# Kernel tuning notes

Measured on AMD Instinct MI355X. Metric: run time of the kernel, lower is better.

## Reference

```python
import jax, jax.numpy as jnp
import numpy as np

EMBED = 768; HEADS = 12; MLP = 3072
WL_IN = 4        # activation bits (signed)
WL_W = 4         # weight bits (bit-sliced into 1-bit RRAM cells)
ADC = 5          # ADC precision for each analog partial sum
SUBARRAY = 128   # crossbar subArray rows
ONOFF = 10.0     # conductance on/off ratio
VARI = 0.02      # conductance variability
EPS = 1e-5


def _adc_quant(y, bits):
    # Linear ADC quantization over the full observed range.
    ymax = jnp.max(jnp.abs(y))
    step = ymax / (2 ** bits - 1)
    step = jnp.where(step > 0, step, jnp.ones_like(step))
    return jnp.round(y / step) * step


def _qlinear(x, W, b, key):
    # RRAM crossbar simulated linear layer. x: [T, Fin], W: [Fout, Fin].
    upper, lower = 1.0, 1.0 / ONOFF
    T, Fin = x.shape
    Fout = W.shape[0]
    Wlev = 2 ** WL_W - 1
    Xlev = 2 ** (WL_IN - 1) - 1
    # --- weight -> unsigned integer levels -> binary cell conductances ---
    wmax = jnp.max(jnp.abs(W))
    Wdec = jnp.round((W / wmax + 1.0) * 0.5 * Wlev).astype(jnp.int32)   # [Fout,Fin] in [0,Wlev]
    kb = jnp.arange(WL_W)
    wbits = ((Wdec[:, :, None] >> kb) & 1).astype(x.dtype)              # [Fout,Fin,K]
    noise = VARI * jax.random.normal(key, wbits.shape, dtype=x.dtype)   # conductance variability
    cond = (wbits * (upper - lower) + lower) * (1.0 + noise)
    dummy = 0.5 * (upper + lower)                                       # dummy column conductance
    # --- activation -> signed integer -> magnitude bit slices ---
    xmax = jnp.max(jnp.abs(x))
    Xq = jnp.round(x / xmax * Xlev).astype(jnp.int32)
    sgn = jnp.sign(Xq).astype(x.dtype)
    zb = jnp.arange(WL_IN - 1)
    xbits = ((jnp.abs(Xq)[:, :, None] >> zb) & 1).astype(x.dtype) * sgn[:, :, None]  # [T,Fin,Z]
    # --- subArray partitioning along input dim ---
    pad = (-Fin) % SUBARRAY
    if pad:
        xbits = jnp.pad(xbits, ((0, 0), (0, pad), (0, 0)))
        cond = jnp.pad(cond, ((0, 0), (0, pad), (0, 0)))
    nc = (Fin + pad) // SUBARRAY
    xb = xbits.reshape(T, nc, SUBARRAY, WL_IN - 1)
    cb = cond.reshape(Fout, nc, SUBARRAY, WL_W)
    # analog MAC per subarray, per (input bit z, weight cell k)
    partial = jnp.einsum('tcsz,ocsk->tcozk', xb, cb)                    # [T,nc,Fout,Z,K]
    dummyP = dummy * xb.sum(axis=2)                                     # [T,nc,Z]
    partialQ = _adc_quant(partial, ADC)
    dummyQ = _adc_quant(dummyP, ADC)
    net = partialQ - dummyQ[:, :, None, :, None]                        # recenter to signed weights
    scale = (2.0 ** zb)[:, None] * (2.0 ** kb)[None, :]                 # [Z,K] shift-add
    acc = jnp.einsum('tcozk,zk->to', net, scale)
    out = acc * (xmax / Xlev) * (2.0 * wmax / ((upper - lower) * Wlev))
    return out + b


def _layernorm(x, g, b):
    mu = jnp.mean(x, axis=-1, keepdims=True)
    var = jnp.var(x, axis=-1, keepdims=True)
    return (x - mu) * jax.lax.rsqrt(var + EPS) * g + b


def _attention(x, in_w, in_b, out_w, out_b):
    L, N, E = x.shape
    D = E // HEADS
    qkv = x @ in_w.T + in_b                                             # [L,N,3E]
    q, k, v = jnp.split(qkv, 3, axis=-1)
    q = q.reshape(L, N, HEADS, D)
    k = k.reshape(L, N, HEADS, D)
    v = v.reshape(L, N, HEADS, D)
    scores = jnp.einsum('lnhd,mnhd->nhlm', q, k) / jnp.sqrt(jnp.asarray(D, x.dtype))
    attn = jax.nn.softmax(scores, axis=-1)
    ctx = jnp.einsum('nhlm,mnhd->lnhd', attn, v).reshape(L, N, E)
    return ctx @ out_w.T + out_b


def setup_inputs() -> dict:
    key = jax.random.key(0)
    ks = jax.random.split(key, 8)
    s = 0.02
    return {
        'x': jax.random.normal(ks[0], (256, 2, EMBED), jnp.float32),
        'in_proj_w': s * jax.random.normal(ks[1], (3 * EMBED, EMBED), jnp.float32),
        'in_proj_b': jnp.zeros((3 * EMBED,), jnp.float32),
        'out_proj_w': s * jax.random.normal(ks[2], (EMBED, EMBED), jnp.float32),
        'out_proj_b': jnp.zeros((EMBED,), jnp.float32),
        'ln1_g': jnp.ones((EMBED,), jnp.float32),
        'ln1_b': jnp.zeros((EMBED,), jnp.float32),
        'W1': s * jax.random.normal(ks[3], (MLP, EMBED), jnp.float32),
        'b1': jnp.zeros((MLP,), jnp.float32),
        'W2': s * jax.random.normal(ks[4], (EMBED, MLP), jnp.float32),
        'b2': jnp.zeros((EMBED,), jnp.float32),
        'ln2_g': jnp.ones((EMBED,), jnp.float32),
        'ln2_b': jnp.zeros((EMBED,), jnp.float32),
    }


def reference(x, in_proj_w, in_proj_b, out_proj_w, out_proj_b,
              ln1_g, ln1_b, W1, b1, W2, b2, ln2_g, ln2_b):
    L, N, E = x.shape
    a = _attention(x, in_proj_w, in_proj_b, out_proj_w, out_proj_b)
    h = _layernorm(x + a, ln1_g, ln1_b)
    t = h.reshape(L * N, E)
    m = _qlinear(t, W1, b1, jax.random.key(1))
    m = jax.nn.gelu(m, approximate=False)   # torch nn.GELU default = exact erf
    m = _qlinear(m, W2, b2, jax.random.key(2))
    m = m.reshape(L, N, E)
    return _layernorm(h + m, ln2_g, ln2_b)
```

## Files before the change

kernel.cpp:

```cpp
#include <hip/hip_runtime.h>
#include <math.h>
#include <stdint.h>

#define TOK   512
#define EMB   768
#define QKVD  2304
#define NHEAD 12
#define HD    64
#define MLPD  3072
#define SUBA  128

#define OFF_SCAL     0ull
#define OFF_QKV      256ull
#define OFF_SCORES   (OFF_QKV    + 4718592ull)
#define OFF_CTX      (OFF_SCORES + 6291456ull)
#define OFF_H1PRE    (OFF_CTX    + 1572864ull)
#define OFF_H1       (OFF_H1PRE  + 1572864ull)
#define OFF_M1       (OFF_H1     + 1572864ull)
#define OFF_X2       (OFF_M1     + 6291456ull)
#define OFF_M2       (OFF_X2     + 6291456ull)
#define OFF_DQ1      (OFF_M2     + 1572864ull)
#define OFF_DQ2      (OFF_DQ1    + 36864ull)
#define OFF_SUMXB1   (OFF_DQ2    + 147456ull)
#define OFF_SUMXB2   (OFF_SUMXB1 + 36864ull)
#define OFF_WDEC1    (OFF_SUMXB2 + 147456ull)
#define OFF_WDEC2    (OFF_WDEC1  + 2359296ull)
#define OFF_XQT1     (OFF_WDEC2  + 2359296ull)
#define OFF_XQT2     (OFF_XQT1   + 393216ull)
#define OFF_COND1    (OFF_XQT2   + 1572864ull)
#define OFF_COND2    (OFF_COND1  + 37748736ull)
#define WS_NEEDED    (OFF_COND2  + 37748736ull)


typedef float f32x2 __attribute__((ext_vector_type(2)));

__device__ __forceinline__ f32x2 pkfma(f32x2 a, f32x2 b, f32x2 c){
  f32x2 d;
  asm("v_pk_fma_f32 %0, %1, %2, %3" : "=v"(d) : "v"(a), "v"(b), "v"(c));
  return d;
}

__device__ __forceinline__ void blockMaxAtomic(double v, unsigned long long* slot, double* red){
  int tid = threadIdx.x;
  red[tid] = v; __syncthreads();
  for (int st = 128; st > 0; st >>= 1){
    if (tid < st){ double o = red[tid+st]; if (o > red[tid]) red[tid] = o; }
    __syncthreads();
  }
  if (tid == 0) atomicMax(slot, (unsigned long long)__double_as_longlong(red[0]));
}

__device__ __forceinline__ double readSlot(const unsigned long long* s){
  return __longlong_as_double((long long)(*s));
}

__device__ __forceinline__ float xla_exp_f32(float _x){
  float x = fminf(_x, 88.3762626647950f);
  x = fmaxf(x, -88.3762626647949f);
  float m = floorf(fmaf(x, 1.44269504088896341f, 0.5f));
  float r = fmaf(m, -0.6931471805599453f, x);
  float r2 = __fmul_rn(r, r);
  float r3 = __fmul_rn(r2, r);
  float y  = fmaf(1.9875691500e-4f, r, 1.3981999507e-3f);
  float y1 = fmaf(4.1665795894e-2f, r, 1.6666665459e-1f);
  float y2 = __fadd_rn(r, 1.0f);
  y  = fmaf(y, r, 8.3334519073e-3f);
  y1 = fmaf(y1, r, 5.0000001201e-1f);
  y  = fmaf(y, r3, y1);
  y  = fmaf(y, r2, y2);
  int mi = (int)m;
  float two_m = __uint_as_float((unsigned)((mi + 127) << 23));
  float res = __fmul_rn(y, two_m);
  return fmaxf(res, _x);
}

__device__ __forceinline__ float xla_erf_f32(float v){
  float x = fmaxf(fminf(v, 4.0f), -4.0f);
  float x2 = __fmul_rn(x, x);
  float p = fmaf(x2, -2.72614225801306e-10f, 2.77068142495902e-08f);
  p = fmaf(x2, p, -2.10102402082508e-06f);
  p = fmaf(x2, p, -5.69250639462346e-05f);
  p = fmaf(x2, p, -7.34990630326855e-04f);
  p = fmaf(x2, p, -2.95459980854025e-03f);
  p = fmaf(x2, p, -1.60960333262415e-02f);
  p = __fmul_rn(x, p);
  float q = fmaf(x2, -1.45660718464996e-05f, -2.13374055278905e-04f);
  q = fmaf(x2, q, -1.68282697438203e-03f);
  q = fmaf(x2, q, -7.37332916720468e-03f);
  q = fmaf(x2, q, -1.42647390514189e-02f);
  return __fdiv_rn(p, q);
}

__device__ __forceinline__ uint32_t rotl32(uint32_t x, int r){ return (x << r) | (x >> (32 - r)); }

__device__ __forceinline__ void threefry2x32(uint32_t k0, uint32_t k1,
                                             uint32_t x0, uint32_t x1,
                                             uint32_t& o0, uint32_t& o1){
  uint32_t ks2 = k0 ^ k1 ^ 0x1BD11BDAu;
  x0 += k0; x1 += k1;
#define TF_R(r) { x0 += x1; x1 = rotl32(x1, r); x1 ^= x0; }
  TF_R(13) TF_R(15) TF_R(26) TF_R(6)
  x0 += k1; x1 += ks2 + 1u;
  TF_R(17) TF_R(29) TF_R(16) TF_R(24)
  x0 += ks2; x1 += k0 + 2u;
  TF_R(13) TF_R(15) TF_R(26) TF_R(6)
  x0 += k0; x1 += k1 + 3u;
  TF_R(17) TF_R(29) TF_R(16) TF_R(24)
  x0 += k1; x1 += ks2 + 4u;
  TF_R(13) TF_R(15) TF_R(26) TF_R(6)
  x0 += ks2; x1 += k0 + 5u;
#undef TF_R
  o0 = x0; o1 = x1;
}

__device__ float bits_to_noise(uint32_t bits){
  uint32_t fb = (bits >> 9) | 0x3f800000u;
  float f = __uint_as_float(fb);
  f = __fadd_rn(f, -1.0f);
  const float lo = -0.99999994f;
  float u = __fadd_rn(__fmul_rn(f, 2.0f), lo);
  u = fmaxf(lo, u);
  float x  = u;
  float xx = __fmul_rn(x, x);
  float nx = -xx;
  float l1p;
  if (fabsf(nx) < 1e-4f){
    l1p = __fmul_rn(__fadd_rn(__fmul_rn(-0.5f, nx), 1.0f), nx);
  } else {
    float u1 = __fadd_rn(nx, 1.0f);
    l1p = (float)log((double)u1);
  }
  float w = -l1p;
  float p;
  if (w < 5.0f){
    w = __fadd_rn(w, -2.5f);
    p = 2.81022636e-08f;
    p = __fadd_rn(3.43273939e-07f, __fmul_rn(p, w));
    p = __fadd_rn(-3.5233877e-06f,  __fmul_rn(p, w));
    p = __fadd_rn(-4.39150654e-06f, __fmul_rn(p, w));
    p = __fadd_rn(0.00021858087f,   __fmul_rn(p, w));
    p = __fadd_rn(-0.00125372503f,  __fmul_rn(p, w));
    p = __fadd_rn(-0.00417768164f,  __fmul_rn(p, w));
    p = __fadd_rn(0.246640727f,     __fmul_rn(p, w));
    p = __fadd_rn(1.50140941f,      __fmul_rn(p, w));
  } else {
    float sw = __fsqrt_rn(w);
    w = __fadd_rn(sw, -3.0f);
    p = -0.000200214257f;
    p = __fadd_rn(0.000100950558f, __fmul_rn(p, w));
    p = __fadd_rn(0.00134934322f,  __fmul_rn(p, w));
    p = __fadd_rn(-0.00367342844f, __fmul_rn(p, w));
    p = __fadd_rn(0.00573950773f,  __fmul_rn(p, w));
    p = __fadd_rn(-0.0076224613f,  __fmul_rn(p, w));
    p = __fadd_rn(0.00943887047f,  __fmul_rn(p, w));
    p = __fadd_rn(1.00167406f,     __fmul_rn(p, w));
    p = __fadd_rn(2.83297682f,     __fmul_rn(p, w));
  }
  float ei  = __fmul_rn(p, x);
  float nrm = __fmul_rn(1.41421354f, ei);
  return __fmul_rn(0.02f, nrm);
}

__global__ void absmax_f32_k(const float* p, int n, unsigned long long* slot){
  __shared__ double red[256];
  double m = 0.0;
  for (int i = blockIdx.x*256 + threadIdx.x; i < n; i += gridDim.x*256){
    double v = fabs((double)p[i]); if (v > m) m = v;
  }
  blockMaxAtomic(m, slot, red);
}

__global__ void wdec_gen_k(const float* W, int nW, const unsigned long long* wmax_slot,
                           unsigned char* Wdec){
  int i = blockIdx.x*256 + threadIdx.x;
  if (i >= nW) return;
  float wmax = (float)readSlot(wmax_slot);
  float d = __fdiv_rn(W[i], wmax);
  d = __fadd_rn(d, 1.0f);
  d = __fmul_rn(d, 0.5f);
  d = __fmul_rn(d, 15.0f);
  Wdec[i] = (unsigned char)(int)rintf(d);
}

__global__ void cond_gen_k(uint32_t k0, uint32_t k1, const unsigned char* Wdec,
                           unsigned int n4, float* cond){
  unsigned int j = blockIdx.x*256u + threadIdx.x;
  if (j >= n4) return;
  uint32_t o0, o1;
  threefry2x32(k0, k1, 0u, j, o0, o1);
  float nz = bits_to_noise(o0 ^ o1);
  float bit = (float)((Wdec[j >> 2] >> (j & 3)) & 1);
  cond[j] = __fmul_rn(__fadd_rn(__fmul_rn(bit, 0.9f), 0.1f), __fadd_rn(1.0f, nz));
}

#define KTILE 32
__global__ __launch_bounds__(256) void gemm8_k(const float* src, const float* w, const float* bias,
                                               const float* resid, float* out, int N, int K){
  __shared__ float xt[EMB*8];
  __shared__ float wl[256*(KTILE+1)];
  const int tid = threadIdx.x;
  const int j  = blockIdx.x*256 + tid;
  const int t0 = blockIdx.y*8;
  for (int v = tid; v < K*8; v += 256){
    int e = v >> 3, tt = v & 7;
    xt[v] = src[(size_t)(t0+tt)*K + e];
  }
  f32x2 acc[4] = {{0.f,0.f},{0.f,0.f},{0.f,0.f},{0.f,0.f}};
  const int ntile = K / KTILE;
  for (int et = 0; et < ntile; ++et){
    __syncthreads();
    for (int v = tid; v < 256*KTILE; v += 256){
      int r = v >> 5, cc = v & 31;
      wl[r*(KTILE+1) + cc] = w[(size_t)(blockIdx.x*256 + r)*K + et*KTILE + cc];
    }
    __syncthreads();
    for (int ee = 0; ee < KTILE; ++ee){
      float wv = wl[tid*(KTILE+1) + ee];
      f32x2 wv2 = {wv, wv};
      const f32x2* xp = (const f32x2*)&xt[(et*KTILE + ee)*8];
#pragma unroll
      for (int q = 0; q < 4; ++q) acc[q] = pkfma(xp[q], wv2, acc[q]);
    }
  }
  float bv = bias[j];
#pragma unroll
  for (int q = 0; q < 4; ++q){
    float a0 = __fadd_rn(acc[q].x, bv);
    float a1 = __fadd_rn(acc[q].y, bv);
    size_t ta = (size_t)(t0 + q*2), tb = ta + 1;
    if (resid){
      out[ta*N + j] = __fadd_rn(resid[ta*N + j], a0);
      out[tb*N + j] = __fadd_rn(resid[tb*N + j], a1);
    } else {
      out[ta*N + j] = a0;
      out[tb*N + j] = a1;
    }
  }
}

__global__ __launch_bounds__(256) void attn_scores_k(const float* qkv, float* sc){
  __shared__ float kt[64][34];
  int nh = blockIdx.x;
  int n  = nh / NHEAD, h = nh % NHEAD;
  int m0 = blockIdx.y * 32;
  int l  = threadIdx.x;
  for (int v = threadIdx.x; v < 32*64; v += 256){
    int mm = v >> 6, d = v & 63;
    kt[d][mm] = qkv[(size_t)((m0+mm)*2 + n)*QKVD + EMB + h*HD + d];
  }
  __syncthreads();
  f32x2 acc[16];
#pragma unroll
  for (int i = 0; i < 16; ++i) acc[i] = {0.f,0.f};
  const float* qrow = qkv + (size_t)(l*2 + n)*QKVD + h*HD;
  for (int d = 0; d < HD; ++d){
    float qv = qrow[d];
    f32x2 q2 = {qv, qv};
    const f32x2* kp = (const f32x2*)&kt[d][0];
#pragma unroll
    for (int i = 0; i < 16; ++i) acc[i] = pkfma(q2, kp[i], acc[i]);
  }
  float* srow = sc + ((size_t)nh*256 + l)*256 + m0;
#pragma unroll
  for (int i = 0; i < 16; ++i){
    srow[2*i]   = __fdiv_rn(acc[i].x, 8.0f);
    srow[2*i+1] = __fdiv_rn(acc[i].y, 8.0f);
  }
}

__global__ void softmax_rows_k(float* sc){
  int row = blockIdx.x*256 + threadIdx.x;
  if (row >= 24*256) return;
  float* p = sc + (size_t)row*256;
  float mx = p[0];
  for (int m = 1; m < 256; ++m) mx = fmaxf(mx, p[m]);
  for (int m = 0; m < 256; ++m) p[m] = xla_exp_f32(__fsub_rn(p[m], mx));
  float s = 0.0f;
  for (int m = 0; m < 256; ++m) s = __fadd_rn(s, p[m]);
  for (int m = 0; m < 256; ++m) p[m] = __fdiv_rn(p[m], s);
}

__global__ void attn_ctx_k(const float* sc, const float* qkv, float* ctx){
  int idx = blockIdx.x*256 + threadIdx.x;
  int t = idx / 384, i2 = idx % 384;
  int i = i2*2;
  int l = t >> 1, n = t & 1, h = i >> 6;
  const float* arow = sc + ((size_t)(n*NHEAD + h)*256 + l)*256;
  f32x2 acc = {0.f,0.f};
  for (int m = 0; m < 256; ++m){
    float av = arow[m];
    f32x2 a2 = {av, av};
    f32x2 v2 = *(const f32x2*)&qkv[(size_t)(m*2 + n)*QKVD + 1536 + i];
    acc = pkfma(a2, v2, acc);
  }
  ctx[(size_t)t*EMB + i]     = acc.x;
  ctx[(size_t)t*EMB + i + 1] = acc.y;
}

__global__ void ln_rows_k(const float* in, const float* g, const float* b, float* out){
  int t = blockIdx.x*256 + threadIdx.x;
  if (t >= TOK) return;
  const float* p = in + (size_t)t*EMB;
  float s = 0.0f;
  for (int e = 0; e < EMB; ++e) s = __fadd_rn(s, p[e]);
  float mu = __fdiv_rn(s, 768.0f);
  float s2 = 0.0f;
  for (int e = 0; e < EMB; ++e){
    float d = __fsub_rn(p[e], mu);
    s2 = __fadd_rn(s2, __fmul_rn(d, d));
  }
  float var = __fdiv_rn(s2, 768.0f);
  float rs = __fdiv_rn(1.0f, __fsqrt_rn(__fadd_rn(var, 1e-5f)));
  for (int e = 0; e < EMB; ++e){
    float d = __fsub_rn(p[e], mu);
    out[(size_t)t*EMB + e] = __fadd_rn(__fmul_rn(__fmul_rn(d, rs), g[e]), b[e]);
  }
}

__global__ void final_ln_rows_k(const float* h1, const float* m2T, const float* g, const float* b, float* out){
  int t = blockIdx.x*256 + threadIdx.x;
  if (t >= TOK) return;
  const float* p = h1 + (size_t)t*EMB;
  float s = 0.0f;
  for (int e = 0; e < EMB; ++e) s = __fadd_rn(s, __fadd_rn(p[e], m2T[(size_t)e*TOK + t]));
  float mu = __fdiv_rn(s, 768.0f);
  float s2 = 0.0f;
  for (int e = 0; e < EMB; ++e){
    float d = __fsub_rn(__fadd_rn(p[e], m2T[(size_t)e*TOK + t]), mu);
    s2 = __fadd_rn(s2, __fmul_rn(d, d));
  }
  float var = __fdiv_rn(s2, 768.0f);
  float rs = __fdiv_rn(1.0f, __fsqrt_rn(__fadd_rn(var, 1e-5f)));
  for (int e = 0; e < EMB; ++e){
    float d = __fsub_rn(__fadd_rn(p[e], m2T[(size_t)e*TOK + t]), mu);
    out[(size_t)t*EMB + e] = __fadd_rn(__fmul_rn(__fmul_rn(d, rs), g[e]), b[e]);
  }
}

__global__ void quantx_k(const float* val , const unsigned long long* xmax_slot,
                         int Fin, signed char* XqT2){
  int idx = blockIdx.x*256 + threadIdx.x;
  if (idx >= TOK*Fin) return;
  int t = idx / Fin, e = idx % Fin;
  float xmax = (float)readSlot(xmax_slot);
  float u = __fmul_rn(__fdiv_rn(val[idx], xmax), 7.0f);
  XqT2[((size_t)(e >> 7)*TOK + t)*SUBA + (e & 127)] = (signed char)(int)rintf(u);
}

__global__ void quantxT_k(const float* valT , const unsigned long long* xmax_slot,
                          int Fin, signed char* XqT2){
  int idx = blockIdx.x*256 + threadIdx.x;
  if (idx >= TOK*Fin) return;
  int i = idx / TOK, t = idx % TOK;
  float xmax = (float)readSlot(xmax_slot);
  float u = __fmul_rn(__fdiv_rn(valT[idx], xmax), 7.0f);
  XqT2[((size_t)(i >> 7)*TOK + t)*SUBA + (i & 127)] = (signed char)(int)rintf(u);
}

__global__ void sumxb_k(const signed char* XqT2, int NC, int* sumxb, unsigned long long* dmax_slot){
  int idx = blockIdx.x*256 + threadIdx.x;
  if (idx >= TOK*NC) return;
  int t = idx / NC, c = idx % NC;
  const signed char* row = XqT2 + ((size_t)c*TOK + t)*SUBA;
  int n0 = 0, n1 = 0, n2 = 0;
  for (int s = 0; s < SUBA; ++s){
    int q = row[s];
    int a = q < 0 ? -q : q;
    int sg = (q > 0) - (q < 0);
    n0 += (a & 1) * sg; n1 += ((a >> 1) & 1) * sg; n2 += ((a >> 2) & 1) * sg;
  }
  sumxb[idx*3 + 0] = n0; sumxb[idx*3 + 1] = n1; sumxb[idx*3 + 2] = n2;
  float d0 = fabsf(__fmul_rn(0.55f, (float)n0));
  float d1 = fabsf(__fmul_rn(0.55f, (float)n1));
  float d2 = fabsf(__fmul_rn(0.55f, (float)n2));
  float m = fmaxf(d0, fmaxf(d1, d2));
  atomicMax(dmax_slot, (unsigned long long)__double_as_longlong((double)m));
}

__global__ void dummyq_k(const int* sumxb, int NC, const unsigned long long* dmax_slot, float* dqT){
  int idx = blockIdx.x*256 + threadIdx.x;
  if (idx >= TOK*NC*3) return;
  int t = idx / (NC*3);
  int r = idx % (NC*3);
  int c = r / 3, z = r % 3;
  float dmax = (float)readSlot(dmax_slot);
  float step = __fdiv_rn(dmax, 31.0f);
  if (!(step > 0.0f)) step = 1.0f;
  float P = __fmul_rn(0.55f, (float)sumxb[idx]);
  dqT[((size_t)c*3 + z)*TOK + t] = __fmul_rn(rintf(__fdiv_rn(P, step)), step);
}

template<int OTILE, bool P2, int CCHUNK>
__global__ __launch_bounds__(256) void qlin_k(const signed char* XqT2, const float* cond_g,
                                              const float* dqT, const float* bias,
                                              int Fin, int NC,
                                              unsigned long long* ymax_slot,
                                              const unsigned long long* xmax_slot,
                                              const unsigned long long* wmax_slot,
                                              float* outT){
  __shared__ float condL[OTILE*SUBA*4];
  __shared__ double red[256];
  const int tid = threadIdx.x;
  const int o0 = blockIdx.x*OTILE;
  const int t0 = blockIdx.y*256;
  const int t  = t0 + tid;
  const int c0 = P2 ? 0 : blockIdx.z*CCHUNK;
  const int cEnd = P2 ? NC : (c0 + CCHUNK);

  float step = 1.0f, lmax = 0.0f;
  if (P2){
    float ymax = (float)readSlot(ymax_slot);
    step = __fdiv_rn(ymax, 31.0f);
    if (!(step > 0.0f)) step = 1.0f;
  }

  f32x2 acc[OTILE][6];
  f32x2 netsum[OTILE][6];
  if (P2){
#pragma unroll
    for (int o = 0; o < OTILE; ++o)
#pragma unroll
      for (int r = 0; r < 6; ++r) netsum[o][r] = (f32x2){0.f, 0.f};
  }

#pragma unroll
  for (int u = 0; u < OTILE/2; ++u){
    int v = tid + u*256, o = v >> 7, r = v & 127;
    ((float4*)condL)[v] = ((const float4*)cond_g)[(size_t)(o0+o)*Fin + (size_t)c0*SUBA + r];
  }
  __syncthreads();

  for (int c = c0; c < cEnd; ++c){
    const uint32_t* xrow = (const uint32_t*)(XqT2 + ((size_t)c*TOK + t)*SUBA);
    uint32_t xg[8];
#pragma unroll
    for (int u = 0; u < 8; ++u) xg[u] = xrow[u];

    float4 pf[OTILE/2];
    const bool havePF = (c + 1 < cEnd);
    if (havePF){
#pragma unroll
      for (int u = 0; u < OTILE/2; ++u){
        int v = tid + u*256, o = v >> 7, r = v & 127;
        pf[u] = ((const float4*)cond_g)[(size_t)(o0+o)*Fin + (size_t)(c+1)*SUBA + r];
      }
    }

#pragma unroll
    for (int o = 0; o < OTILE; ++o)
#pragma unroll
      for (int r = 0; r < 6; ++r) acc[o][r] = (f32x2){0.f, 0.f};

    for (int g = 0; g < 4; ++g){
      uint32_t xn[8];
      if (g < 3){
#pragma unroll
        for (int u = 0; u < 8; ++u) xn[u] = xrow[(g+1)*8 + u];
      }
      const float* condG = condL + g*32*4;
#pragma unroll
      for (int u = 0; u < 8; ++u){
        uint32_t w = xg[u];
#pragma unroll
        for (int bb = 0; bb < 4; ++bb){
          int sl = u*4 + bb;
          int q = (int)(signed char)(w >> (8*bb));
          int a = q < 0 ? -q : q;
          int i0 = a & 1, i1 = (a >> 1) & 1, i2 = (a >> 2) & 1;
          if (q < 0){ i0 = -i0; i1 = -i1; i2 = -i2; }
          float f0 = (float)i0, f1 = (float)i1, f2 = (float)i2;
          f32x2 b0 = {f0, f0}, b1 = {f1, f1}, b2 = {f2, f2};
#pragma unroll
          for (int o = 0; o < OTILE; ++o){
            const f32x2* cp = (const f32x2*)&condG[(o*SUBA + sl)*4];
            f32x2 c01 = cp[0], c23 = cp[1];
            acc[o][0] = pkfma(b0, c01, acc[o][0]);
            acc[o][1] = pkfma(b0, c23, acc[o][1]);
            acc[o][2] = pkfma(b1, c01, acc[o][2]);
            acc[o][3] = pkfma(b1, c23, acc[o][3]);
            acc[o][4] = pkfma(b2, c01, acc[o][4]);
            acc[o][5] = pkfma(b2, c23, acc[o][5]);
          }
        }
      }
      if (g < 3){
#pragma unroll
        for (int u = 0; u < 8; ++u) xg[u] = xn[u];
      }
    }

    if (P2){
      float dqv[3];
#pragma unroll
      for (int z = 0; z < 3; ++z) dqv[z] = dqT[((size_t)c*3 + z)*TOK + t];
#pragma unroll
      for (int o = 0; o < OTILE; ++o)
#pragma unroll
        for (int z = 0; z < 3; ++z)
#pragma unroll
          for (int kp = 0; kp < 2; ++kp){
            f32x2 av = acc[o][z*2 + kp];
            float pq0 = __fmul_rn(rintf(__fdiv_rn(av.x, step)), step);
            float pq1 = __fmul_rn(rintf(__fdiv_rn(av.y, step)), step);
            netsum[o][z*2+kp].x = __fadd_rn(netsum[o][z*2+kp].x, __fsub_rn(pq0, dqv[z]));
            netsum[o][z*2+kp].y = __fadd_rn(netsum[o][z*2+kp].y, __fsub_rn(pq1, dqv[z]));
          }
    } else {
#pragma unroll
      for (int o = 0; o < OTILE; ++o)
#pragma unroll
        for (int r = 0; r < 6; ++r){
          lmax = fmaxf(lmax, fabsf(acc[o][r].x));
          lmax = fmaxf(lmax, fabsf(acc[o][r].y));
        }
    }

    __syncthreads();
    if (havePF){
#pragma unroll
      for (int u = 0; u < OTILE/2; ++u)
        ((float4*)condL)[tid + u*256] = pf[u];
      __syncthreads();
    }
  }

  if (P2){
    float xmax = (float)readSlot(xmax_slot);
    float wmax = (float)readSlot(wmax_slot);
    float A = __fdiv_rn(xmax, 7.0f);
    float B = __fdiv_rn(__fmul_rn(2.0f, wmax), 13.5f);
#pragma unroll
    for (int o = 0; o < OTILE; ++o){
      float tot = 0.0f;
#pragma unroll
      for (int z = 0; z < 3; ++z)
#pragma unroll
        for (int k = 0; k < 4; ++k){
          f32x2 ns = netsum[o][z*2 + (k >> 1)];
          float nv = (k & 1) ? ns.y : ns.x;
          tot = __fadd_rn(tot, __fmul_rn(nv, (float)(1 << (z + k))));
        }
      float outv = __fadd_rn(__fmul_rn(__fmul_rn(tot, A), B), bias[o0+o]);
      outT[(size_t)(o0+o)*TOK + t] = outv;
    }
  } else {
    blockMaxAtomic((double)lmax, ymax_slot, red);
  }
}

__global__ void gelu_absmax_k(const float* m1, int n, float* x2, unsigned long long* xmax_slot){
  __shared__ double red[256];
  double m = 0.0;
  for (int i = blockIdx.x*256 + threadIdx.x; i < n; i += gridDim.x*256){
    float v = m1[i];
    float t1 = __fdiv_rn(v, 1.4142135623730951f);
    float e = xla_erf_f32(t1);
    float s = __fadd_rn(e, 1.0f);
    float g = __fdiv_rn(__fmul_rn(v, s), 2.0f);
    x2[i] = g;
    double a = fabs((double)g); if (a > m) m = a;
  }
  blockMaxAtomic(m, xmax_slot, red);
}

extern "C" void kernel_launch(void* const* d_in, const int* in_sizes, int n_in,
                              void* d_out, int out_size, void* d_ws, size_t ws_size,
                              hipStream_t stream){
  if (ws_size < WS_NEEDED) return;
  const float* x      = (const float*)d_in[0];
  const float* in_w   = (const float*)d_in[1];
  const float* in_b   = (const float*)d_in[2];
  const float* out_w  = (const float*)d_in[3];
  const float* out_b  = (const float*)d_in[4];
  const float* ln1_g  = (const float*)d_in[5];
  const float* ln1_b  = (const float*)d_in[6];
  const float* W1     = (const float*)d_in[7];
  const float* b1     = (const float*)d_in[8];
  const float* W2     = (const float*)d_in[9];
  const float* b2     = (const float*)d_in[10];
  const float* ln2_g  = (const float*)d_in[11];
  const float* ln2_b  = (const float*)d_in[12];

  char* ws = (char*)d_ws;
  unsigned long long* scal = (unsigned long long*)(ws + OFF_SCAL);
  float* qkv    = (float*)(ws + OFF_QKV);
  float* scores = (float*)(ws + OFF_SCORES);
  float* ctx    = (float*)(ws + OFF_CTX);
  float* h1pre  = (float*)(ws + OFF_H1PRE);
  float* h1     = (float*)(ws + OFF_H1);
  float* m1     = (float*)(ws + OFF_M1);
  float* x2     = (float*)(ws + OFF_X2);
  float* m2     = (float*)(ws + OFF_M2);
  float* dq1    = (float*)(ws + OFF_DQ1);
  float* dq2    = (float*)(ws + OFF_DQ2);
  int*   sumxb1 = (int*)(ws + OFF_SUMXB1);
  int*   sumxb2 = (int*)(ws + OFF_SUMXB2);
  unsigned char* wdec1 = (unsigned char*)(ws + OFF_WDEC1);
  unsigned char* wdec2 = (unsigned char*)(ws + OFF_WDEC2);
  signed char* xqt1 = (signed char*)(ws + OFF_XQT1);
  signed char* xqt2 = (signed char*)(ws + OFF_XQT2);
  float* cond1 = (float*)(ws + OFF_COND1);
  float* cond2 = (float*)(ws + OFF_COND2);

  hipMemsetAsync(scal, 0, 64, stream);

  absmax_f32_k<<<1024,256,0,stream>>>(W1, MLPD*EMB, scal+0);
  absmax_f32_k<<<1024,256,0,stream>>>(W2, EMB*MLPD, scal+1);
  wdec_gen_k<<<9216,256,0,stream>>>(W1, MLPD*EMB, scal+0, wdec1);
  wdec_gen_k<<<9216,256,0,stream>>>(W2, EMB*MLPD, scal+1, wdec2);
  cond_gen_k<<<36864,256,0,stream>>>(0u, 1u, wdec1, 9437184u, cond1);
  cond_gen_k<<<36864,256,0,stream>>>(0u, 2u, wdec2, 9437184u, cond2);

  gemm8_k<<<dim3(9,64),256,0,stream>>>(x, in_w, in_b, nullptr, qkv, QKVD, EMB);
  attn_scores_k<<<dim3(24,8),256,0,stream>>>(qkv, scores);
  softmax_rows_k<<<24,256,0,stream>>>(scores);
  attn_ctx_k<<<768,256,0,stream>>>(scores, qkv, ctx);
  gemm8_k<<<dim3(3,64),256,0,stream>>>(ctx, out_w, out_b, x, h1pre, EMB, EMB);
  ln_rows_k<<<2,256,0,stream>>>(h1pre, ln1_g, ln1_b, h1);

  absmax_f32_k<<<1024,256,0,stream>>>(h1, TOK*EMB, scal+2);
  quantx_k<<<(TOK*EMB+255)/256,256,0,stream>>>(h1, scal+2, EMB, xqt1);
  sumxb_k<<<(TOK*6+255)/256,256,0,stream>>>(xqt1, 6, sumxb1, scal+4);
  dummyq_k<<<(TOK*6*3+255)/256,256,0,stream>>>(sumxb1, 6, scal+4, dq1);
  qlin_k<4,false,3><<<dim3(MLPD/4,2,2),256,0,stream>>>(xqt1, cond1, nullptr, nullptr,
                                                       EMB, 6, scal+3, scal+2, scal+0, nullptr);
  qlin_k<4,true,1><<<dim3(MLPD/4,2),256,0,stream>>>(xqt1, cond1, dq1, b1,
                                                    EMB, 6, scal+3, scal+2, scal+0, m1);

  gelu_absmax_k<<<6144,256,0,stream>>>(m1, TOK*MLPD, x2, scal+5);
  quantxT_k<<<(TOK*MLPD+255)/256,256,0,stream>>>(x2, scal+5, MLPD, xqt2);
  sumxb_k<<<(TOK*24+255)/256,256,0,stream>>>(xqt2, 24, sumxb2, scal+7);
  dummyq_k<<<(TOK*24*3+255)/256,256,0,stream>>>(sumxb2, 24, scal+7, dq2);
  qlin_k<4,false,6><<<dim3(EMB/4,2,4),256,0,stream>>>(xqt2, cond2, nullptr, nullptr,
                                                      MLPD, 24, scal+6, scal+5, scal+1, nullptr);
  qlin_k<4,true,1><<<dim3(EMB/4,2),256,0,stream>>>(xqt2, cond2, dq2, b2,
                                                   MLPD, 24, scal+6, scal+5, scal+1, m2);

  final_ln_rows_k<<<2,256,0,stream>>>(h1, m2, ln2_g, ln2_b, (float*)d_out);
}
```

Measured before the change: 3.201 ms.

## Pre-encode activation bit slices, prefetch across chunks, shrink P2 tile

Quantized activations are now stored as packed signed 2-bit fields per bit slice, so the qlin inner loop decodes them with shifts instead of abs/sign/branch logic. The next chunk's activation row is prefetched across chunk boundaries, and the P2 pass no longer reserves the unused reduction shared array. The second-layer P2 pass switches to a 2-output tile with twice as many blocks, and pkfma now uses a builtin instead of inline asm. Together these aim to cut integer ALU work in the hot loop and raise occupancy, at the risk of the compiler emitting scalar FMAs rather than packed ones.

Measured after the change: 2.881 ms. 10.0% less time.

```diff
diff --git a/kernel.cpp b/kernel.cpp
--- a/kernel.cpp
+++ b/kernel.cpp
@@ -35,9 +35,11 @@
 typedef float f32x2 __attribute__((ext_vector_type(2)));
 
 __device__ __forceinline__ f32x2 pkfma(f32x2 a, f32x2 b, f32x2 c){
-  f32x2 d;
-  asm("v_pk_fma_f32 %0, %1, %2, %3" : "=v"(d) : "v"(a), "v"(b), "v"(c));
-  return d;
+#if __has_builtin(__builtin_elementwise_fma)
+  return __builtin_elementwise_fma(a, b, c);
+#else
+  f32x2 r; r.x = fmaf(a.x, b.x, c.x); r.y = fmaf(a.y, b.y, c.y); return r;
+#endif
 }
 
 __device__ __forceinline__ void blockMaxAtomic(double v, unsigned long long* slot, double* red){
@@ -337,37 +339,44 @@
   }
 }
 
+__device__ __forceinline__ unsigned char encode_q(int q){
+  int a = q < 0 ? -q : q;
+  int s0 = a & 1, s1 = (a >> 1) & 1, s2 = (a >> 2) & 1;
+  if (q < 0){ s0 = -s0; s1 = -s1; s2 = -s2; }
+  return (unsigned char)((s0 & 3) | ((s1 & 3) << 2) | ((s2 & 3) << 4));
+}
+
 __global__ void quantx_k(const float* val , const unsigned long long* xmax_slot,
-                         int Fin, signed char* XqT2){
+                         int Fin, unsigned char* XqT2){
   int idx = blockIdx.x*256 + threadIdx.x;
   if (idx >= TOK*Fin) return;
   int t = idx / Fin, e = idx % Fin;
   float xmax = (float)readSlot(xmax_slot);
   float u = __fmul_rn(__fdiv_rn(val[idx], xmax), 7.0f);
-  XqT2[((size_t)(e >> 7)*TOK + t)*SUBA + (e & 127)] = (signed char)(int)rintf(u);
+  XqT2[((size_t)(e >> 7)*TOK + t)*SUBA + (e & 127)] = encode_q((int)rintf(u));
 }
 
 __global__ void quantxT_k(const float* valT , const unsigned long long* xmax_slot,
-                          int Fin, signed char* XqT2){
+                          int Fin, unsigned char* XqT2){
   int idx = blockIdx.x*256 + threadIdx.x;
   if (idx >= TOK*Fin) return;
   int i = idx / TOK, t = idx % TOK;
   float xmax = (float)readSlot(xmax_slot);
   float u = __fmul_rn(__fdiv_rn(valT[idx], xmax), 7.0f);
-  XqT2[((size_t)(i >> 7)*TOK + t)*SUBA + (i & 127)] = (signed char)(int)rintf(u);
-}
-
-__global__ void sumxb_k(const signed char* XqT2, int NC, int* sumxb, unsigned long long* dmax_slot){
+  XqT2[((size_t)(i >> 7)*TOK + t)*SUBA + (i & 127)] = encode_q((int)rintf(u));
+}
+
+__global__ void sumxb_k(const unsigned char* XqT2, int NC, int* sumxb, unsigned long long* dmax_slot){
   int idx = blockIdx.x*256 + threadIdx.x;
   if (idx >= TOK*NC) return;
   int t = idx / NC, c = idx % NC;
-  const signed char* row = XqT2 + ((size_t)c*TOK + t)*SUBA;
+  const unsigned char* row = XqT2 + ((size_t)c*TOK + t)*SUBA;
   int n0 = 0, n1 = 0, n2 = 0;
   for (int s = 0; s < SUBA; ++s){
-    int q = row[s];
-    int a = q < 0 ? -q : q;
-    int sg = (q > 0) - (q < 0);
-    n0 += (a & 1) * sg; n1 += ((a >> 1) & 1) * sg; n2 += ((a >> 2) & 1) * sg;
+    int e = (int)row[s];
+    n0 += ((int)((unsigned)e << 30)) >> 30;
+    n1 += ((int)((unsigned)e << 28)) >> 30;
+    n2 += ((int)((unsigned)e << 26)) >> 30;
   }
   sumxb[idx*3 + 0] = n0; sumxb[idx*3 + 1] = n1; sumxb[idx*3 + 2] = n2;
   float d0 = fabsf(__fmul_rn(0.55f, (float)n0));
@@ -391,7 +400,7 @@
 }
 
 template<int OTILE, bool P2, int CCHUNK>
-__global__ __launch_bounds__(256) void qlin_k(const signed char* XqT2, const float* cond_g,
+__global__ __launch_bounds__(256) void qlin_k(const unsigned char* XqT2, const float* cond_g,
                                               const float* dqT, const float* bias,
                                               int Fin, int NC,
                                               unsigned long long* ymax_slot,
@@ -399,7 +408,7 @@
                                               const unsigned long long* wmax_slot,
                                               float* outT){
   __shared__ float condL[OTILE*SUBA*4];
-  __shared__ double red[256];
+  __shared__ double red[P2 ? 1 : 256];
   const int tid = threadIdx.x;
   const int o0 = blockIdx.x*OTILE;
   const int t0 = blockIdx.y*256;
@@ -430,15 +439,18 @@
   }
   __syncthreads();
 
+  const uint32_t* xrow = (const uint32_t*)(XqT2 + ((size_t)c0*TOK + t)*SUBA);
+  uint32_t xg[8];
+#pragma unroll
+  for (int u = 0; u < 8; ++u) xg[u] = xrow[u];
+
   for (int c = c0; c < cEnd; ++c){
-    const uint32_t* xrow = (const uint32_t*)(XqT2 + ((size_t)c*TOK + t)*SUBA);
-    uint32_t xg[8];
-#pragma unroll
-    for (int u = 0; u < 8; ++u) xg[u] = xrow[u];
+    const bool haveNextC = (c + 1 < cEnd);
+    const uint32_t* xrow_next = haveNextC
+      ? (const uint32_t*)(XqT2 + ((size_t)(c+1)*TOK + t)*SUBA) : xrow;
 
     float4 pf[OTILE/2];
-    const bool havePF = (c + 1 < cEnd);
-    if (havePF){
+    if (haveNextC){
 #pragma unroll
       for (int u = 0; u < OTILE/2; ++u){
         int v = tid + u*256, o = v >> 7, r = v & 127;
@@ -453,10 +465,9 @@
 
     for (int g = 0; g < 4; ++g){
       uint32_t xn[8];
-      if (g < 3){
-#pragma unroll
-        for (int u = 0; u < 8; ++u) xn[u] = xrow[(g+1)*8 + u];
-      }
+      const uint32_t* nsrc = (g < 3) ? (xrow + (g+1)*8) : xrow_next;
+#pragma unroll
+      for (int u = 0; u < 8; ++u) xn[u] = nsrc[u];
       const float* condG = condL + g*32*4;
 #pragma unroll
       for (int u = 0; u < 8; ++u){
@@ -464,11 +475,11 @@
 #pragma unroll
         for (int bb = 0; bb < 4; ++bb){
           int sl = u*4 + bb;
-          int q = (int)(signed char)(w >> (8*bb));
-          int a = q < 0 ? -q : q;
-          int i0 = a & 1, i1 = (a >> 1) & 1, i2 = (a >> 2) & 1;
-          if (q < 0){ i0 = -i0; i1 = -i1; i2 = -i2; }
-          float f0 = (float)i0, f1 = (float)i1, f2 = (float)i2;
+          int base = bb*8;
+          int b0i = ((int)(w << (30 - base))) >> 30;
+          int b1i = ((int)(w << (28 - base))) >> 30;
+          int b2i = ((int)(w << (26 - base))) >> 30;
+          float f0 = (float)b0i, f1 = (float)b1i, f2 = (float)b2i;
           f32x2 b0 = {f0, f0}, b1 = {f1, f1}, b2 = {f2, f2};
 #pragma unroll
           for (int o = 0; o < OTILE; ++o){
@@ -483,11 +494,10 @@
           }
         }
       }
-      if (g < 3){
-#pragma unroll
-        for (int u = 0; u < 8; ++u) xg[u] = xn[u];
-      }
-    }
+#pragma unroll
+      for (int u = 0; u < 8; ++u) xg[u] = xn[u];
+    }
+    xrow = xrow_next;
 
     if (P2){
       float dqv[3];
@@ -516,7 +526,7 @@
     }
 
     __syncthreads();
-    if (havePF){
+    if (haveNextC){
 #pragma unroll
       for (int u = 0; u < OTILE/2; ++u)
         ((float4*)condL)[tid + u*256] = pf[u];
@@ -597,8 +607,8 @@
   int*   sumxb2 = (int*)(ws + OFF_SUMXB2);
   unsigned char* wdec1 = (unsigned char*)(ws + OFF_WDEC1);
   unsigned char* wdec2 = (unsigned char*)(ws + OFF_WDEC2);
-  signed char* xqt1 = (signed char*)(ws + OFF_XQT1);
-  signed char* xqt2 = (signed char*)(ws + OFF_XQT2);
+  unsigned char* xqt1 = (unsigned char*)(ws + OFF_XQT1);
+  unsigned char* xqt2 = (unsigned char*)(ws + OFF_XQT2);
   float* cond1 = (float*)(ws + OFF_COND1);
   float* cond2 = (float*)(ws + OFF_COND2);
 
@@ -633,7 +643,7 @@
   dummyq_k<<<(TOK*24*3+255)/256,256,0,stream>>>(sumxb2, 24, scal+7, dq2);
   qlin_k<4,false,6><<<dim3(EMB/4,2,4),256,0,stream>>>(xqt2, cond2, nullptr, nullptr,
                                                       MLPD, 24, scal+6, scal+5, scal+1, nullptr);
-  qlin_k<4,true,1><<<dim3(EMB/4,2),256,0,stream>>>(xqt2, cond2, dq2, b2,
+  qlin_k<2,true,1><<<dim3(EMB/2,2),256,0,stream>>>(xqt2, cond2, dq2, b2,
                                                    MLPD, 24, scal+6, scal+5, scal+1, m2);
 
   final_ln_rows_k<<<2,256,0,stream>>>(h1, m2, ln2_g, ln2_b, (float*)d_out);
```
